# Kernel tuning notes

Measured on AMD Instinct MI355X. Metric: run time of the kernel, lower is better.

The kernel has to match this reference:

```python
import jax, jax.numpy as jnp
import numpy as np
import math

N_HEADS = 8

def setup_inputs() -> dict:
    key = jax.random.key(0)
    qkv = jax.random.normal(key, (4, 1536, 2048), dtype=jnp.float32)
    return {"qkv": qkv}

def reference(qkv):
    bs, width, length = qkv.shape
    ch = width // (3 * N_HEADS)
    # reshape to [bs*n_heads, 3*ch, length] then split into q, k, v
    qkv_h = qkv.reshape(bs * N_HEADS, 3 * ch, length)
    q = qkv_h[:, :ch]
    k = qkv_h[:, ch:2 * ch]
    v = qkv_h[:, 2 * ch:]
    scale = 1.0 / math.sqrt(math.sqrt(ch))
    # scores: [B*H, T, S]
    weight = jnp.einsum('bct,bcs->bts', q * scale, k * scale)
    weight = jax.nn.softmax(weight.astype(jnp.float32), axis=-1).astype(weight.dtype)
    a = jnp.einsum('bts,bcs->bct', weight, v)  # [B*H, ch, T]
    return a.reshape(bs, N_HEADS * ch, length)
```

## Files before the change

### kernel.cpp

```cpp
#include <hip/hip_runtime.h>
#include <hip/hip_bf16.h>

typedef __attribute__((ext_vector_type(8))) short bf16x8;
typedef __attribute__((ext_vector_type(8))) unsigned short u16x8;
typedef __attribute__((ext_vector_type(4))) float f32x4;
typedef __attribute__((ext_vector_type(16))) float f32x16;

#define SEQ 2048
#define BT 128
#define BS 64
#define NBH 32
#define QSCALE 0.1803368801111204f

#if __has_builtin(__builtin_amdgcn_exp2f)
#define EXP2(x) __builtin_amdgcn_exp2f(x)
#else
#define EXP2(x) exp2f(x)
#endif

__device__ __forceinline__ unsigned short bfc(float f) {
  union { __hip_bfloat16 h; unsigned short u; } v;
  v.h = __float2bfloat16(f);
  return v.u;
}

__device__ __forceinline__ void gl_lds16(const void* g, void* l) {
  __builtin_amdgcn_global_load_lds((__attribute__((address_space(1))) void*)g,
                                   (__attribute__((address_space(3))) void*)l, 16, 0, 0);
}

__global__ __launch_bounds__(256)
void prep_kernel(const float* __restrict__ qkv, unsigned short* __restrict__ ws) {
  const int tid = threadIdx.x;
  const int b = blockIdx.x;
  if (b < 4096) {
    int gid = b * 256 + tid;
    int sec = gid >> 19;
    int r = gid & 524287;
    int bh = r >> 14;
    int rr = r & 16383;
    int cc = rr >> 11;
    int t = rr & 2047;
    const float* src = qkv + ((size_t)(bh >> 3) * 1536 + (bh & 7) * 192 + sec * 64 + cc * 8) * SEQ + t;
    const float scale = sec ? 1.0f : QSCALE;
    u16x8 o;
    #pragma unroll
    for (int e = 0; e < 8; ++e) o[e] = bfc(src[(size_t)e * SEQ] * scale);
    unsigned short* dst = ws + ((size_t)sec * NBH * SEQ + (size_t)bh * SEQ + t) * 64;
    *(u16x8*)(dst + ((cc ^ (t & 7)) * 8)) = o;
  } else {
    int cid = (b - 4096) * 256 + tid;
    int bh = cid >> 14;
    int rr = cid & 16383;
    int c = rr >> 8;
    int cc = rr & 255;
    int grp = cc >> 3, sub = cc & 7;
    const float* src = qkv + ((size_t)(bh >> 3) * 1536 + (bh & 7) * 192 + 128 + c) * SEQ + cc * 8;
    float4 a = *(const float4*)(src);
    float4 bv = *(const float4*)(src + 4);
    u16x8 o;
    o[0] = bfc(a.x); o[1] = bfc(a.y); o[2] = bfc(a.z); o[3] = bfc(a.w);
    o[4] = bfc(bv.x); o[5] = bfc(bv.y); o[6] = bfc(bv.z); o[7] = bfc(bv.w);
    unsigned short* dst = ws + (size_t)2 * NBH * SEQ * 64 +
                          ((size_t)bh * 64 + c) * SEQ + grp * 64 + ((sub ^ (c & 7)) * 8);
    *(u16x8*)dst = o;
  }
}

__global__ __launch_bounds__(256, 2)
void attn_main(const unsigned short* __restrict__ ws, float* __restrict__ out) {
  const int bid = blockIdx.x;
  const int bh = (bid & 7) + 8 * ((bid >> 3) >> 4);
  const int tile = (bid >> 3) & 15;
  const int t0 = tile * BT;

  const unsigned short* Qws = ws + ((size_t)bh * SEQ + t0) * 64;
  const unsigned short* Kws = ws + (size_t)NBH * SEQ * 64 + (size_t)bh * SEQ * 64;
  const unsigned short* Vws = ws + (size_t)2 * NBH * SEQ * 64 + (size_t)bh * 64 * SEQ;
  float* __restrict__ outb = out + (size_t)bh * 64 * SEQ;

  __shared__ __align__(16) unsigned short QP[BT * 64];
  __shared__ __align__(16) unsigned short Kt[2][BS * 64];
  __shared__ __align__(16) unsigned short Vt[2][BS * 64];

  const int tid = threadIdx.x;
  const int w = tid >> 6;
  const int l = tid & 63;
  const int lw = l & 31;
  const int h = l >> 5;
  const int sw = lw & 7;

  #pragma unroll
  for (int i = 0; i < 4; ++i)
    gl_lds16(Qws + (size_t)(tid + i * 256) * 8, &QP[(tid + i * 256) * 8]);
  gl_lds16(Kws + (size_t)tid * 8, &Kt[0][tid * 8]);
  gl_lds16(Kws + (size_t)(tid + 256) * 8, &Kt[0][(tid + 256) * 8]);
  gl_lds16(Vws + (size_t)(tid >> 3) * SEQ + (tid & 7) * 8, &Vt[0][tid * 8]);
  gl_lds16(Vws + (size_t)((tid >> 3) + 32) * SEQ + (tid & 7) * 8, &Vt[0][(tid + 256) * 8]);
  __syncthreads();

  bf16x8 qB[4];
  {
    const int rloc = w * 32 + lw;
    #pragma unroll
    for (int kc = 0; kc < 4; ++kc)
      qB[kc] = *(const bf16x8*)&QP[rloc * 64 + (((2 * kc + h) ^ sw) * 8)];
  }

  f32x16 zero16;
  #pragma unroll
  for (int i = 0; i < 16; ++i) zero16[i] = 0.f;
  bf16x8 onesB;
  #pragma unroll
  for (int i = 0; i < 8; ++i) onesB[i] = (short)0x3F80;

  f32x16 accO[2]; f32x16 psum;
  accO[0] = zero16; accO[1] = zero16; psum = zero16;

  int cur = 0;
  #pragma unroll 1
  for (int it = 0; it < SEQ / BS; ++it) {
    const int s1 = (it + 1) & 31;
    gl_lds16(Kws + (size_t)s1 * 4096 + tid * 8, &Kt[cur ^ 1][tid * 8]);
    gl_lds16(Kws + (size_t)s1 * 4096 + (tid + 256) * 8, &Kt[cur ^ 1][(tid + 256) * 8]);
    gl_lds16(Vws + (size_t)(tid >> 3) * SEQ + s1 * 64 + (tid & 7) * 8, &Vt[cur ^ 1][tid * 8]);
    gl_lds16(Vws + (size_t)((tid >> 3) + 32) * SEQ + s1 * 64 + (tid & 7) * 8, &Vt[cur ^ 1][(tid + 256) * 8]);

    const unsigned short* kb = Kt[cur];
    const unsigned short* vb = Vt[cur];

    f32x16 accS[2];
    #pragma unroll
    for (int ms = 0; ms < 2; ++ms) {
      #pragma unroll
      for (int kc = 0; kc < 4; ++kc) {
        bf16x8 ka = *(const bf16x8*)&kb[(32 * ms + lw) * 64 + (((2 * kc + h) ^ sw) * 8)];
        accS[ms] = __builtin_amdgcn_mfma_f32_32x32x16_bf16(ka, qB[kc], kc ? accS[ms] : zero16, 0, 0, 0);
      }
    }

    #pragma unroll
    for (int ms = 0; ms < 2; ++ms)
      #pragma unroll
      for (int r = 0; r < 16; ++r) accS[ms][r] = EXP2(accS[ms][r]);

    unsigned int pk[2][8];
    #pragma unroll
    for (int ms = 0; ms < 2; ++ms)
      #pragma unroll
      for (int wd = 0; wd < 8; ++wd)
        asm("v_cvt_pk_bf16_f32 %0, %1, %2"
            : "=v"(pk[ms][wd]) : "v"(accS[ms][2 * wd]), "v"(accS[ms][2 * wd + 1]));

    bf16x8 pA[4];
    #pragma unroll
    for (int ks = 0; ks < 4; ++ks) {
      const int a = ks & 1, ms = ks >> 1;
      unsigned int x0 = pk[ms][4 * a + 0], y0 = pk[ms][4 * a + 2];
      unsigned int x1 = pk[ms][4 * a + 1], y1 = pk[ms][4 * a + 3];
      asm("v_permlane32_swap_b32 %0, %1" : "+v"(x0), "+v"(y0));
      asm("v_permlane32_swap_b32 %0, %1" : "+v"(x1), "+v"(y1));
      union { unsigned int u[4]; bf16x8 v; } uu;
      uu.u[0] = x0; uu.u[1] = x1; uu.u[2] = y0; uu.u[3] = y1;
      pA[ks] = uu.v;
    }

    #pragma unroll
    for (int ks = 0; ks < 4; ++ks)
      psum = __builtin_amdgcn_mfma_f32_32x32x16_bf16(pA[ks], onesB, psum, 0, 0, 0);

    #pragma unroll
    for (int ch = 0; ch < 2; ++ch) {
      #pragma unroll
      for (int ks = 0; ks < 4; ++ks) {
        bf16x8 vB = *(const bf16x8*)&vb[(32 * ch + lw) * 64 + (((2 * ks + h) ^ sw) * 8)];
        accO[ch] = __builtin_amdgcn_mfma_f32_32x32x16_bf16(pA[ks], vB, accO[ch], 0, 0, 0);
      }
    }

    __syncthreads();
    cur ^= 1;
  }

  {
    float linv[16];
    #pragma unroll
    for (int r = 0; r < 16; ++r) linv[r] = 1.0f / psum[r];
    #pragma unroll
    for (int ch = 0; ch < 2; ++ch) {
      #pragma unroll
      for (int r = 0; r < 16; ++r) {
        const int tg = t0 + w * 32 + (r & 3) + 8 * (r >> 2) + 4 * h;
        outb[(size_t)(32 * ch + lw) * SEQ + tg] = accO[ch][r] * linv[r];
      }
    }
  }
}

#define PAD 72
__device__ __forceinline__ unsigned short f2bf(float f) {
  union { float f; unsigned u; } v; v.f = f;
  return (unsigned short)((v.u + 0x7fffu + ((v.u >> 16) & 1u)) >> 16);
}

__global__ __launch_bounds__(512, 4)
void qkv_attn_fallback(const float* __restrict__ qkv, float* __restrict__ out) {
  const int bid = blockIdx.x;
  const int xcd = bid & 7;
  const int slot = bid >> 3;
  const int bh = xcd + 8 * (slot >> 4);
  const int tile = slot & 15;
  const int t0 = tile * BT;

  const float* __restrict__ base = qkv + (size_t)((bh >> 3) * 1536 + (bh & 7) * 192) * SEQ;
  const float* __restrict__ qg = base;
  const float* __restrict__ kg = base + 64 * SEQ;
  const float* __restrict__ vg = base + 128 * SEQ;
  float* __restrict__ outb = out + (size_t)bh * 64 * SEQ;

  __shared__ __align__(16) unsigned short Qt[BT * PAD];
  __shared__ __align__(16) unsigned short Kt[BS * PAD];
  __shared__ __align__(16) unsigned short Vt[64 * PAD];
  __shared__ __align__(16) unsigned short Pl[BT * PAD];

  const int tid = threadIdx.x;
  const int w = tid >> 6;
  const int l = tid & 63;
  const int lr = l & 15;
  const int g = l >> 4;

  {
    const int cb = tid >> 5, tb = tid & 31;
    const int c0 = cb * 4, tt0 = tb * 4;
    const float* p = qg + c0 * SEQ + t0 + tt0;
    float4 r0 = *(const float4*)(p);
    float4 r1 = *(const float4*)(p + SEQ);
    float4 r2 = *(const float4*)(p + 2 * SEQ);
    float4 r3 = *(const float4*)(p + 3 * SEQ);
    const float s = 0.125f;
    ushort4 w0 = { f2bf(r0.x*s), f2bf(r1.x*s), f2bf(r2.x*s), f2bf(r3.x*s) };
    ushort4 w1 = { f2bf(r0.y*s), f2bf(r1.y*s), f2bf(r2.y*s), f2bf(r3.y*s) };
    ushort4 w2 = { f2bf(r0.z*s), f2bf(r1.z*s), f2bf(r2.z*s), f2bf(r3.z*s) };
    ushort4 w3 = { f2bf(r0.w*s), f2bf(r1.w*s), f2bf(r2.w*s), f2bf(r3.w*s) };
    *(ushort4*)&Qt[(tt0 + 0) * PAD + c0] = w0;
    *(ushort4*)&Qt[(tt0 + 1) * PAD + c0] = w1;
    *(ushort4*)&Qt[(tt0 + 2) * PAD + c0] = w2;
    *(ushort4*)&Qt[(tt0 + 3) * PAD + c0] = w3;
  }
  __syncthreads();

  bf16x8 qB0 = *(const bf16x8*)&Qt[(w * 16 + lr) * PAD + g * 8];
  bf16x8 qB1 = *(const bf16x8*)&Qt[(w * 16 + lr) * PAD + g * 8 + 32];

  f32x4 pv[4];
  #pragma unroll
  for (int i = 0; i < 4; ++i) pv[i] = (f32x4){0.f, 0.f, 0.f, 0.f};
  float mrun = -1e30f;
  float lsum = 0.f;

  for (int s0 = 0; s0 < SEQ; s0 += BS) {
    __syncthreads();
    {
      const int cb = tid >> 4, sb = tid & 15;
      const int c0 = cb * 2, sl = sb * 4;
      const float* p0 = kg + c0 * SEQ + s0 + sl;
      float4 a0 = *(const float4*)(p0);
      float4 a1 = *(const float4*)(p0 + SEQ);
      ushort2 y0 = { f2bf(a0.x), f2bf(a1.x) };
      ushort2 y1 = { f2bf(a0.y), f2bf(a1.y) };
      ushort2 y2 = { f2bf(a0.z), f2bf(a1.z) };
      ushort2 y3 = { f2bf(a0.w), f2bf(a1.w) };
      *(ushort2*)&Kt[(sl + 0) * PAD + c0] = y0;
      *(ushort2*)&Kt[(sl + 1) * PAD + c0] = y1;
      *(ushort2*)&Kt[(sl + 2) * PAD + c0] = y2;
      *(ushort2*)&Kt[(sl + 3) * PAD + c0] = y3;
    }
    {
      const int c = tid >> 3;
      const int sq = (tid & 7) * 8;
      const float* p0 = vg + c * SEQ + s0 + sq;
      float4 b0 = *(const float4*)(p0);
      float4 b1 = *(const float4*)(p0 + 4);
      ushort4 z0 = { f2bf(b0.x), f2bf(b0.y), f2bf(b0.z), f2bf(b0.w) };
      ushort4 z1 = { f2bf(b1.x), f2bf(b1.y), f2bf(b1.z), f2bf(b1.w) };
      *(ushort4*)&Vt[c * PAD + sq] = z0;
      *(ushort4*)&Vt[c * PAD + sq + 4] = z1;
    }
    __syncthreads();

    f32x4 acc[4];
    #pragma unroll
    for (int i = 0; i < 4; ++i) acc[i] = (f32x4){0.f, 0.f, 0.f, 0.f};
    #pragma unroll
    for (int ch = 0; ch < 2; ++ch) {
      bf16x8 qb = ch ? qB1 : qB0;
      #pragma unroll
      for (int sub = 0; sub < 4; ++sub) {
        bf16x8 ka = *(const bf16x8*)&Kt[(sub * 16 + lr) * PAD + g * 8 + 32 * ch];
        acc[sub] = __builtin_amdgcn_mfma_f32_16x16x32_bf16(ka, qb, acc[sub], 0, 0, 0);
      }
    }

    float pmax = -1e30f;
    #pragma unroll
    for (int sub = 0; sub < 4; ++sub)
      #pragma unroll
      for (int r = 0; r < 4; ++r) pmax = fmaxf(pmax, acc[sub][r]);
    pmax = fmaxf(pmax, __shfl_xor(pmax, 16));
    pmax = fmaxf(pmax, __shfl_xor(pmax, 32));
    const float mnew = fmaxf(mrun, pmax);
    const float alpha = __expf(mrun - mnew);
    float rsum = 0.f;
    #pragma unroll
    for (int sub = 0; sub < 4; ++sub) {
      #pragma unroll
      for (int r = 0; r < 4; ++r) {
        float p = __expf(acc[sub][r] - mnew);
        acc[sub][r] = p;
        rsum += p;
      }
    }
    rsum += __shfl_xor(rsum, 16);
    rsum += __shfl_xor(rsum, 32);
    lsum = lsum * alpha + rsum;
    mrun = mnew;

    #pragma unroll
    for (int sub = 0; sub < 4; ++sub) {
      ushort4 pw = { f2bf(acc[sub][0]), f2bf(acc[sub][1]), f2bf(acc[sub][2]), f2bf(acc[sub][3]) };
      *(ushort4*)&Pl[(w * 16 + lr) * PAD + sub * 16 + g * 4] = pw;
    }

    {
      const int sbase = (l & 48) + g * 4;
      #pragma unroll
      for (int r = 0; r < 4; ++r) {
        float ar = __shfl(alpha, sbase + r, 64);
        #pragma unroll
        for (int cs = 0; cs < 4; ++cs) pv[cs][r] *= ar;
      }
    }

    bf16x8 pA0 = *(const bf16x8*)&Pl[(w * 16 + lr) * PAD + g * 8];
    bf16x8 pA1 = *(const bf16x8*)&Pl[(w * 16 + lr) * PAD + g * 8 + 32];
    #pragma unroll
    for (int cs = 0; cs < 4; ++cs) {
      bf16x8 v0 = *(const bf16x8*)&Vt[(cs * 16 + lr) * PAD + g * 8];
      bf16x8 v1 = *(const bf16x8*)&Vt[(cs * 16 + lr) * PAD + g * 8 + 32];
      pv[cs] = __builtin_amdgcn_mfma_f32_16x16x32_bf16(pA0, v0, pv[cs], 0, 0, 0);
      pv[cs] = __builtin_amdgcn_mfma_f32_16x16x32_bf16(pA1, v1, pv[cs], 0, 0, 0);
    }
  }

  {
    const int sbase = (l & 48) + g * 4;
    float linv[4];
    #pragma unroll
    for (int r = 0; r < 4; ++r) linv[r] = 1.0f / __shfl(lsum, sbase + r, 64);
    #pragma unroll
    for (int cs = 0; cs < 4; ++cs) {
      #pragma unroll
      for (int r = 0; r < 4; ++r) {
        outb[(cs * 16 + lr) * SEQ + t0 + w * 16 + g * 4 + r] = pv[cs][r] * linv[r];
      }
    }
  }
}

extern "C" void kernel_launch(void* const* d_in, const int* in_sizes, int n_in,
                              void* d_out, int out_size, void* d_ws, size_t ws_size,
                              hipStream_t stream) {
  const float* qkv = (const float*)d_in[0];
  float* out = (float*)d_out;
  const size_t need = (size_t)3 * NBH * SEQ * 64 * sizeof(unsigned short);
  if (ws_size >= need) {
    unsigned short* ws = (unsigned short*)d_ws;
    prep_kernel<<<dim3(6144), dim3(256), 0, stream>>>(qkv, ws);
    attn_main<<<dim3(512), dim3(256), 0, stream>>>(ws, out);
  } else {
    qkv_attn_fallback<<<dim3(512), dim3(512), 0, stream>>>(qkv, out);
  }
}
```

Before: 66.25 us.

## Enlarge attention tile to 256 queries with split-KV waves and LDS reduction

The main attention kernel now processes 256 query rows per block with 512 threads. Each of the 8 waves handles 64 query rows and one half of a 128-key step, and each K/V fragment read from LDS feeds two MFMAs, so K/V reuse doubles. The two key-halves are combined at the end through a shared-memory reduction of the output and row-sum accumulators. The costs are fewer blocks (256 on a 256-CU part), one block per CU with 96KB of LDS, higher register pressure and an extra reduction step.

```diff
diff --git a/kernel.cpp b/kernel.cpp
--- a/kernel.cpp
+++ b/kernel.cpp
@@ -7,8 +7,6 @@
 typedef __attribute__((ext_vector_type(16))) float f32x16;
 
 #define SEQ 2048
-#define BT 128
-#define BS 64
 #define NBH 32
 #define QSCALE 0.1803368801111204f
 
@@ -67,24 +65,27 @@
   }
 }
 
-__global__ __launch_bounds__(256, 2)
+__global__ __launch_bounds__(512, 1)
 void attn_main(const unsigned short* __restrict__ ws, float* __restrict__ out) {
   const int bid = blockIdx.x;
-  const int bh = (bid & 7) + 8 * ((bid >> 3) >> 4);
-  const int tile = (bid >> 3) & 15;
-  const int t0 = tile * BT;
+  const int bh = (bid & 7) + 8 * ((bid >> 3) >> 3);
+  const int tile = (bid >> 3) & 7;
+  const int t0 = tile * 256;
 
   const unsigned short* Qws = ws + ((size_t)bh * SEQ + t0) * 64;
   const unsigned short* Kws = ws + (size_t)NBH * SEQ * 64 + (size_t)bh * SEQ * 64;
   const unsigned short* Vws = ws + (size_t)2 * NBH * SEQ * 64 + (size_t)bh * 64 * SEQ;
   float* __restrict__ outb = out + (size_t)bh * 64 * SEQ;
 
-  __shared__ __align__(16) unsigned short QP[BT * 64];
-  __shared__ __align__(16) unsigned short Kt[2][BS * 64];
-  __shared__ __align__(16) unsigned short Vt[2][BS * 64];
+  __shared__ __align__(16) char smem[98304];
+  unsigned short* QP = (unsigned short*)smem;
+  unsigned short* KtB = (unsigned short*)(smem + 32768);
+  unsigned short* VtB = (unsigned short*)(smem + 65536);
 
   const int tid = threadIdx.x;
   const int w = tid >> 6;
+  const int ts = w & 3;
+  const int sh = w >> 2;
   const int l = tid & 63;
   const int lw = l & 31;
   const int h = l >> 5;
@@ -92,19 +93,24 @@
 
   #pragma unroll
   for (int i = 0; i < 4; ++i)
-    gl_lds16(Qws + (size_t)(tid + i * 256) * 8, &QP[(tid + i * 256) * 8]);
-  gl_lds16(Kws + (size_t)tid * 8, &Kt[0][tid * 8]);
-  gl_lds16(Kws + (size_t)(tid + 256) * 8, &Kt[0][(tid + 256) * 8]);
-  gl_lds16(Vws + (size_t)(tid >> 3) * SEQ + (tid & 7) * 8, &Vt[0][tid * 8]);
-  gl_lds16(Vws + (size_t)((tid >> 3) + 32) * SEQ + (tid & 7) * 8, &Vt[0][(tid + 256) * 8]);
+    gl_lds16(Qws + (size_t)(tid + i * 512) * 8, &QP[(tid + i * 512) * 8]);
+  gl_lds16(Kws + (size_t)tid * 8, &KtB[tid * 8]);
+  gl_lds16(Kws + (size_t)(tid + 512) * 8, &KtB[(tid + 512) * 8]);
+  {
+    int q = tid;       int c = q >> 4, g2 = (q >> 3) & 1, j = q & 7;
+    gl_lds16(Vws + (size_t)c * SEQ + g2 * 64 + j * 8, &VtB[q * 8]);
+    q = tid + 512;     c = q >> 4;     g2 = (q >> 3) & 1; j = q & 7;
+    gl_lds16(Vws + (size_t)c * SEQ + g2 * 64 + j * 8, &VtB[q * 8]);
+  }
   __syncthreads();
 
-  bf16x8 qB[4];
-  {
-    const int rloc = w * 32 + lw;
+  bf16x8 qB[2][4];
+  #pragma unroll
+  for (int tsub = 0; tsub < 2; ++tsub) {
+    const int rloc = ts * 64 + tsub * 32 + lw;
     #pragma unroll
     for (int kc = 0; kc < 4; ++kc)
-      qB[kc] = *(const bf16x8*)&QP[rloc * 64 + (((2 * kc + h) ^ sw) * 8)];
+      qB[tsub][kc] = *(const bf16x8*)&QP[rloc * 64 + (((2 * kc + h) ^ sw) * 8)];
   }
 
   f32x16 zero16;
@@ -114,67 +120,88 @@
   #pragma unroll
   for (int i = 0; i < 8; ++i) onesB[i] = (short)0x3F80;
 
-  f32x16 accO[2]; f32x16 psum;
-  accO[0] = zero16; accO[1] = zero16; psum = zero16;
+  f32x16 accO[2][2];
+  f32x16 psum[2];
+  accO[0][0] = zero16; accO[0][1] = zero16;
+  accO[1][0] = zero16; accO[1][1] = zero16;
+  psum[0] = zero16; psum[1] = zero16;
 
   int cur = 0;
   #pragma unroll 1
-  for (int it = 0; it < SEQ / BS; ++it) {
-    const int s1 = (it + 1) & 31;
-    gl_lds16(Kws + (size_t)s1 * 4096 + tid * 8, &Kt[cur ^ 1][tid * 8]);
-    gl_lds16(Kws + (size_t)s1 * 4096 + (tid + 256) * 8, &Kt[cur ^ 1][(tid + 256) * 8]);
-    gl_lds16(Vws + (size_t)(tid >> 3) * SEQ + s1 * 64 + (tid & 7) * 8, &Vt[cur ^ 1][tid * 8]);
-    gl_lds16(Vws + (size_t)((tid >> 3) + 32) * SEQ + s1 * 64 + (tid & 7) * 8, &Vt[cur ^ 1][(tid + 256) * 8]);
-
-    const unsigned short* kb = Kt[cur];
-    const unsigned short* vb = Vt[cur];
-
-    f32x16 accS[2];
+  for (int it = 0; it < SEQ / 128; ++it) {
+    const int s1 = (it + 1) & 15;
+    {
+      const unsigned short* kn = Kws + (size_t)s1 * 8192;
+      unsigned short* kd = KtB + (cur ^ 1) * 8192;
+      gl_lds16(kn + (size_t)tid * 8, &kd[tid * 8]);
+      gl_lds16(kn + (size_t)(tid + 512) * 8, &kd[(tid + 512) * 8]);
+      unsigned short* vd = VtB + (cur ^ 1) * 8192;
+      int q = tid;     int c = q >> 4, g2 = (q >> 3) & 1, j = q & 7;
+      gl_lds16(Vws + (size_t)c * SEQ + (2 * s1 + g2) * 64 + j * 8, &vd[q * 8]);
+      q = tid + 512;   c = q >> 4;     g2 = (q >> 3) & 1; j = q & 7;
+      gl_lds16(Vws + (size_t)c * SEQ + (2 * s1 + g2) * 64 + j * 8, &vd[q * 8]);
+    }
+
+    const unsigned short* kb = KtB + cur * 8192;
+    const unsigned short* vb = VtB + cur * 8192;
+
+    f32x16 accS[2][2];
     #pragma unroll
     for (int ms = 0; ms < 2; ++ms) {
       #pragma unroll
       for (int kc = 0; kc < 4; ++kc) {
-        bf16x8 ka = *(const bf16x8*)&kb[(32 * ms + lw) * 64 + (((2 * kc + h) ^ sw) * 8)];
-        accS[ms] = __builtin_amdgcn_mfma_f32_32x32x16_bf16(ka, qB[kc], kc ? accS[ms] : zero16, 0, 0, 0);
+        bf16x8 ka = *(const bf16x8*)&kb[(sh * 64 + 32 * ms + lw) * 64 + (((2 * kc + h) ^ sw) * 8)];
+        #pragma unroll
+        for (int tsub = 0; tsub < 2; ++tsub)
+          accS[ms][tsub] = __builtin_amdgcn_mfma_f32_32x32x16_bf16(
+              ka, qB[tsub][kc], kc ? accS[ms][tsub] : zero16, 0, 0, 0);
       }
     }
 
     #pragma unroll
     for (int ms = 0; ms < 2; ++ms)
       #pragma unroll
-      for (int r = 0; r < 16; ++r) accS[ms][r] = EXP2(accS[ms][r]);
-
-    unsigned int pk[2][8];
-    #pragma unroll
-    for (int ms = 0; ms < 2; ++ms)
-      #pragma unroll
-      for (int wd = 0; wd < 8; ++wd)
-        asm("v_cvt_pk_bf16_f32 %0, %1, %2"
-            : "=v"(pk[ms][wd]) : "v"(accS[ms][2 * wd]), "v"(accS[ms][2 * wd + 1]));
-
-    bf16x8 pA[4];
-    #pragma unroll
-    for (int ks = 0; ks < 4; ++ks) {
-      const int a = ks & 1, ms = ks >> 1;
-      unsigned int x0 = pk[ms][4 * a + 0], y0 = pk[ms][4 * a + 2];
-      unsigned int x1 = pk[ms][4 * a + 1], y1 = pk[ms][4 * a + 3];
-      asm("v_permlane32_swap_b32 %0, %1" : "+v"(x0), "+v"(y0));
-      asm("v_permlane32_swap_b32 %0, %1" : "+v"(x1), "+v"(y1));
-      union { unsigned int u[4]; bf16x8 v; } uu;
-      uu.u[0] = x0; uu.u[1] = x1; uu.u[2] = y0; uu.u[3] = y1;
-      pA[ks] = uu.v;
-    }
-
-    #pragma unroll
-    for (int ks = 0; ks < 4; ++ks)
-      psum = __builtin_amdgcn_mfma_f32_32x32x16_bf16(pA[ks], onesB, psum, 0, 0, 0);
+      for (int tsub = 0; tsub < 2; ++tsub)
+        #pragma unroll
+        for (int r = 0; r < 16; ++r) accS[ms][tsub][r] = EXP2(accS[ms][tsub][r]);
+
+    bf16x8 pA[2][4];
+    #pragma unroll
+    for (int tsub = 0; tsub < 2; ++tsub) {
+      #pragma unroll
+      for (int ms = 0; ms < 2; ++ms) {
+        unsigned int pk[8];
+        #pragma unroll
+        for (int wd = 0; wd < 8; ++wd)
+          asm("v_cvt_pk_bf16_f32 %0, %1, %2"
+              : "=v"(pk[wd]) : "v"(accS[ms][tsub][2 * wd]), "v"(accS[ms][tsub][2 * wd + 1]));
+        #pragma unroll
+        for (int a = 0; a < 2; ++a) {
+          unsigned int x0 = pk[4 * a + 0], y0 = pk[4 * a + 2];
+          unsigned int x1 = pk[4 * a + 1], y1 = pk[4 * a + 3];
+          asm("v_permlane32_swap_b32 %0, %1" : "+v"(x0), "+v"(y0));
+          asm("v_permlane32_swap_b32 %0, %1" : "+v"(x1), "+v"(y1));
+          union { unsigned int u[4]; bf16x8 v; } uu;
+          uu.u[0] = x0; uu.u[1] = x1; uu.u[2] = y0; uu.u[3] = y1;
+          pA[tsub][2 * ms + a] = uu.v;
+        }
+      }
+    }
+
+    #pragma unroll
+    for (int tsub = 0; tsub < 2; ++tsub)
+      #pragma unroll
+      for (int ks = 0; ks < 4; ++ks)
+        psum[tsub] = __builtin_amdgcn_mfma_f32_32x32x16_bf16(pA[tsub][ks], onesB, psum[tsub], 0, 0, 0);
 
     #pragma unroll
     for (int ch = 0; ch < 2; ++ch) {
       #pragma unroll
       for (int ks = 0; ks < 4; ++ks) {
-        bf16x8 vB = *(const bf16x8*)&vb[(32 * ch + lw) * 64 + (((2 * ks + h) ^ sw) * 8)];
-        accO[ch] = __builtin_amdgcn_mfma_f32_32x32x16_bf16(pA[ks], vB, accO[ch], 0, 0, 0);
+        bf16x8 vB = *(const bf16x8*)&vb[(32 * ch + lw) * 128 + sh * 64 + (((2 * ks + h) ^ sw) * 8)];
+        #pragma unroll
+        for (int tsub = 0; tsub < 2; ++tsub)
+          accO[tsub][ch] = __builtin_amdgcn_mfma_f32_32x32x16_bf16(pA[tsub][ks], vB, accO[tsub][ch], 0, 0, 0);
       }
     }
 
@@ -182,22 +209,46 @@
     cur ^= 1;
   }
 
-  {
-    float linv[16];
-    #pragma unroll
-    for (int r = 0; r < 16; ++r) linv[r] = 1.0f / psum[r];
-    #pragma unroll
-    for (int ch = 0; ch < 2; ++ch) {
-      #pragma unroll
-      for (int r = 0; r < 16; ++r) {
-        const int tg = t0 + w * 32 + (r & 3) + 8 * (r >> 2) + 4 * h;
-        outb[(size_t)(32 * ch + lw) * SEQ + tg] = accO[ch][r] * linv[r];
+  float* cO = (float*)smem;
+  float* cP = (float*)(smem + 65536);
+  if (sh == 1) {
+    #pragma unroll
+    for (int tsub = 0; tsub < 2; ++tsub) {
+      #pragma unroll
+      for (int ch = 0; ch < 2; ++ch)
+        #pragma unroll
+        for (int r = 0; r < 16; ++r)
+          cO[ts * 4096 + (tsub * 2 + ch) * 1024 + r * 64 + l] = accO[tsub][ch][r];
+      #pragma unroll
+      for (int r = 0; r < 16; ++r)
+        cP[ts * 2048 + tsub * 1024 + r * 64 + l] = psum[tsub][r];
+    }
+  }
+  __syncthreads();
+  if (sh == 0) {
+    #pragma unroll
+    for (int tsub = 0; tsub < 2; ++tsub) {
+      #pragma unroll
+      for (int r = 0; r < 16; ++r)
+        psum[tsub][r] += cP[ts * 2048 + tsub * 1024 + r * 64 + l];
+      float linv[16];
+      #pragma unroll
+      for (int r = 0; r < 16; ++r) linv[r] = 1.0f / psum[tsub][r];
+      #pragma unroll
+      for (int ch = 0; ch < 2; ++ch) {
+        #pragma unroll
+        for (int r = 0; r < 16; ++r) {
+          float v = accO[tsub][ch][r] + cO[ts * 4096 + (tsub * 2 + ch) * 1024 + r * 64 + l];
+          const int tg = t0 + ts * 64 + tsub * 32 + (r & 3) + 8 * (r >> 2) + 4 * h;
+          outb[(size_t)(32 * ch + lw) * SEQ + tg] = v * linv[r];
+        }
       }
     }
   }
 }
 
 #define PAD 72
+#define BTF 128
 __device__ __forceinline__ unsigned short f2bf(float f) {
   union { float f; unsigned u; } v; v.f = f;
   return (unsigned short)((v.u + 0x7fffu + ((v.u >> 16) & 1u)) >> 16);
@@ -210,7 +261,7 @@
   const int slot = bid >> 3;
   const int bh = xcd + 8 * (slot >> 4);
   const int tile = slot & 15;
-  const int t0 = tile * BT;
+  const int t0 = tile * BTF;
 
   const float* __restrict__ base = qkv + (size_t)((bh >> 3) * 1536 + (bh & 7) * 192) * SEQ;
   const float* __restrict__ qg = base;
@@ -218,10 +269,10 @@
   const float* __restrict__ vg = base + 128 * SEQ;
   float* __restrict__ outb = out + (size_t)bh * 64 * SEQ;
 
-  __shared__ __align__(16) unsigned short Qt[BT * PAD];
-  __shared__ __align__(16) unsigned short Kt[BS * PAD];
+  __shared__ __align__(16) unsigned short Qt[BTF * PAD];
+  __shared__ __align__(16) unsigned short Kt[64 * PAD];
   __shared__ __align__(16) unsigned short Vt[64 * PAD];
-  __shared__ __align__(16) unsigned short Pl[BT * PAD];
+  __shared__ __align__(16) unsigned short Pl[BTF * PAD];
 
   const int tid = threadIdx.x;
   const int w = tid >> 6;
@@ -258,7 +309,7 @@
   float mrun = -1e30f;
   float lsum = 0.f;
 
-  for (int s0 = 0; s0 < SEQ; s0 += BS) {
+  for (int s0 = 0; s0 < SEQ; s0 += 64) {
     __syncthreads();
     {
       const int cb = tid >> 4, sb = tid & 15;
@@ -376,7 +427,7 @@
   if (ws_size >= need) {
     unsigned short* ws = (unsigned short*)d_ws;
     prep_kernel<<<dim3(6144), dim3(256), 0, stream>>>(qkv, ws);
-    attn_main<<<dim3(512), dim3(256), 0, stream>>>(ws, out);
+    attn_main<<<dim3(256), dim3(512), 0, stream>>>(ws, out);
   } else {
     qkv_attn_fallback<<<dim3(512), dim3(512), 0, stream>>>(qkv, out);
   }
```

New measurement: 58.37 us. 11.9% less time.
